# Optimization experiments

Hardware: AMD Instinct MI355X
Metric: run time of the kernel (lower is better)

Reference implementation:

```python
import jax, jax.numpy as jnp
import numpy as np

N_HEAD = 16
NEG = -1e10


def setup_inputs() -> dict:
    key = jax.random.key(0)
    ks = jax.random.split(key, 10)
    B, T, C = 2, 2048, 1024
    hs = C // N_HEAD
    inv = 1.0 / np.sqrt(C)
    return {
        "x": jax.random.normal(ks[0], (B, T, C), jnp.float32),
        "W1": jax.random.normal(ks[1], (C, C), jnp.float32) * inv,
        "bw1": jnp.zeros((C,), jnp.float32),
        "b1": jnp.zeros((hs,), jnp.float32),
        # original init: uniform(-0.001, 0.001)
        "w2": jax.random.uniform(ks[2], (hs, T), jnp.float32, -0.001, 0.001),
        "b2": jnp.zeros((T,), jnp.float32),
        "Wv": jax.random.normal(ks[3], (C, C), jnp.float32) * inv,
        "bv": jnp.zeros((C,), jnp.float32),
        "Wp": jax.random.normal(ks[4], (C, C), jnp.float32) * inv,
        "bp": jnp.zeros((C,), jnp.float32),
    }


def reference(x, W1, bw1, b1, w2, b2, Wv, bv, Wp, bp):
    B, T, C = x.shape
    nh = N_HEAD
    hs = C // nh
    # factorized synthesizer 'query': (B, nh, T, hs)
    h = (x @ W1 + bw1).reshape(B, T, nh, hs).transpose(0, 2, 1, 3)
    # scores: relu(h + b1) @ w2 + b2  -> (B, nh, T, T)
    att = jnp.einsum('bhtd,dk->bhtk', jax.nn.relu(h + b1), w2[:, :T]) + b2[:T]
    # causal mask then softmax (masked_fill with -1e10, as in original)
    causal = jnp.tril(jnp.ones((T, T), bool))
    att = jnp.where(causal[None, None], att, NEG)
    att = jax.nn.softmax(att, axis=-1)
    # values
    v = (x @ Wv + bv).reshape(B, T, nh, hs).transpose(0, 2, 1, 3)
    y = jnp.einsum('bhtk,bhkd->bhtd', att, v)
    y = y.transpose(0, 2, 1, 3).reshape(B, T, C)
    return y @ Wp + bp
```

## Files before the change

kernel.cpp:

```cpp
#include <hip/hip_runtime.h>
#include <hip/hip_bf16.h>

#define TSEQ 2048
#define CDIM 1024
#define NH 16
#define HS 64

typedef __attribute__((ext_vector_type(8))) short bf16x8;
typedef __attribute__((ext_vector_type(4))) float f32x4;
typedef __attribute__((ext_vector_type(16))) float f32x16;

__device__ inline void gload16(const void* g, void* l) {
    __builtin_amdgcn_global_load_lds((const __attribute__((address_space(1))) void*)g,
                                     (__attribute__((address_space(3))) void*)l, 16, 0, 0);
}
__device__ inline void gload4(const void* g, void* l) {
    __builtin_amdgcn_global_load_lds((const __attribute__((address_space(1))) void*)g,
                                     (__attribute__((address_space(3))) void*)l, 4, 0, 0);
}

__device__ inline unsigned packbf(float a, float b) {
    union { __hip_bfloat162 h; unsigned u; } cv;
    cv.h = __float22bfloat162_rn(make_float2(a, b));
    return cv.u;
}

__global__ __launch_bounds__(256)
void prep(const float* __restrict__ x, __hip_bfloat16* __restrict__ xb, int nx,
          const float* __restrict__ W1, const float* __restrict__ Wv,
          const float* __restrict__ Wp, __hip_bfloat16* __restrict__ o1,
          __hip_bfloat16* __restrict__ o2, __hip_bfloat16* __restrict__ o3,
          const float* __restrict__ w2, __hip_bfloat16* __restrict__ w2t,
          const float* __restrict__ b2, float* __restrict__ bl,
          int nconv, int nt3, int nw2)
{
    __shared__ float t[32][33];
    const int bid = blockIdx.x;
    const int tid = threadIdx.x;

    if (bid < nconv) {
        int i = (bid * 256 + tid) * 4;
        if (i + 3 < nx) {
            float4 v = *(const float4*)(x + i);
            union { ushort4 u; __hip_bfloat16 h[4]; } o;
            o.h[0] = __float2bfloat16(v.x);
            o.h[1] = __float2bfloat16(v.y);
            o.h[2] = __float2bfloat16(v.z);
            o.h[3] = __float2bfloat16(v.w);
            *(ushort4*)((unsigned short*)xb + i) = o.u;
        }
    } else if (bid < nconv + nt3) {
        const int idx = bid - nconv;
        const int z = idx >> 10;
        const int rest = idx & 1023;
        const int by = rest >> 5, bx = rest & 31;
        const float* in = z == 0 ? W1 : (z == 1 ? Wv : Wp);
        __hip_bfloat16* out = z == 0 ? o1 : (z == 1 ? o2 : o3);
        const int tx = tid & 31, ty = tid >> 5;
        const int r0 = by * 32, c0 = bx * 32;
        #pragma unroll
        for (int i = 0; i < 32; i += 8)
            t[ty + i][tx] = in[(size_t)(r0 + ty + i) * CDIM + c0 + tx];
        __syncthreads();
        #pragma unroll
        for (int i = 0; i < 32; i += 8)
            out[(size_t)(c0 + ty + i) * CDIM + r0 + tx] = __float2bfloat16(t[tx][ty + i]);
    } else if (bid < nconv + nt3 + nw2) {
        const int idx = bid - nconv - nt3;
        const int bx = idx & 63, by = idx >> 6;
        const int tx = tid & 31, ty = tid >> 5;
        const int r0 = by * 32, c0 = bx * 32;
        #pragma unroll
        for (int i = 0; i < 32; i += 8)
            t[ty + i][tx] = w2[(size_t)(r0 + ty + i) * TSEQ + c0 + tx];
        __syncthreads();
        #pragma unroll
        for (int i = 0; i < 32; i += 8)
            w2t[(size_t)(c0 + ty + i) * HS + r0 + tx] = __float2bfloat16(t[tx][ty + i]);
    } else {
        const int i = (bid - nconv - nt3 - nw2) * 256 + tid;
        if (i < TSEQ) bl[i] = b2[i] * 1.44269504f;
    }
}

__global__ __launch_bounds__(256, 2)
void gemm_qv(const __hip_bfloat16* __restrict__ X, const __hip_bfloat16* __restrict__ W,
             const float* __restrict__ bw1, const float* __restrict__ b1,
             const float* __restrict__ bv, __hip_bfloat16* __restrict__ Hb,
             __hip_bfloat16* __restrict__ Vblk, int M)
{
    __shared__ __align__(16) __hip_bfloat16 As[128 * 32];
    __shared__ __align__(16) __hip_bfloat16 Bs[128 * 32];
    const int tid = threadIdx.x, wave = tid >> 6, lane = tid & 63;
    const int wr = wave >> 1, wc = wave & 1, l15 = lane & 15, l4 = lane >> 4;
    const int m0 = blockIdx.y * 128, n0 = blockIdx.x * 128;
    const int K = CDIM;
    const int Bb = M >> 11;
    const int srow = wave * 32 + (lane >> 2), scol = (lane & 3) * 8;
    const __hip_bfloat16* xg = X + (size_t)(m0 + srow) * K + scol;
    const __hip_bfloat16* wg = W + (size_t)(n0 + srow) * K + scol;
    __hip_bfloat16* la = &As[wave * 32 * 32];
    __hip_bfloat16* lb = &Bs[wave * 32 * 32];

    f32x4 acc[4][4] = {};
    for (int k0 = 0; k0 < K; k0 += 32) {
        __syncthreads();
        gload16(xg + k0, la);
        gload16(xg + k0 + (size_t)16 * K, la + 16 * 32);
        gload16(wg + k0, lb);
        gload16(wg + k0 + (size_t)16 * K, lb + 16 * 32);
        __syncthreads();
        bf16x8 af[4], bfr[4];
        #pragma unroll
        for (int f = 0; f < 4; f++) af[f]  = *(const bf16x8*)&As[(wr * 64 + f * 16 + l15) * 32 + l4 * 8];
        #pragma unroll
        for (int f = 0; f < 4; f++) bfr[f] = *(const bf16x8*)&Bs[(wc * 64 + f * 16 + l15) * 32 + l4 * 8];
        #pragma unroll
        for (int fr = 0; fr < 4; fr++)
            #pragma unroll
            for (int fc = 0; fc < 4; fc++)
                acc[fr][fc] = __builtin_amdgcn_mfma_f32_16x16x32_bf16(af[fr], bfr[fc], acc[fr][fc], 0, 0, 0);
    }

    const bool isH = (n0 < CDIM);
    const int sl4 = ((l4 & 1) << 1) | (l4 >> 1);
    if (isH) {
        #pragma unroll
        for (int fc = 0; fc < 4; fc++) {
            const int col = n0 + wc * 64 + fc * 16 + l15;
            const float bias = bw1[col] + b1[col & (HS - 1)];
            #pragma unroll
            for (int fr = 0; fr < 4; fr++)
                #pragma unroll
                for (int r = 0; r < 4; r++) {
                    const int row = m0 + wr * 64 + fr * 16 + l4 * 4 + r;
                    const float hv = fmaxf(acc[fr][fc][r] + bias, 0.f) * 1.44269504f;
                    Hb[(size_t)row * CDIM + col] = __float2bfloat16(hv);
                }
        }
    } else {
        const int mt = m0 + wr * 64;
        const int bb = mt >> 11;
        const int ktb = (mt & (TSEQ - 1)) >> 6;
        const int hh = ((n0 - CDIM) + wc * 64) >> 6;
        __hip_bfloat16* tile = Vblk + (((size_t)hh * Bb + bb) * (TSEQ / 64) + ktb) * (HS * 64);
        #pragma unroll
        for (int fc = 0; fc < 4; fc++) {
            const int d = fc * 16 + l15;
            const int c2 = hh * HS + d;
            const float bias = bv[c2];
            #pragma unroll
            for (int fr = 0; fr < 4; fr++) {
                const int tl = fr * 16 + sl4 * 4;
                union { ushort4 u; __hip_bfloat16 h[4]; } o;
                #pragma unroll
                for (int r = 0; r < 4; r++) o.h[r] = __float2bfloat16(acc[fr][fc][r] + bias);
                *(ushort4*)(tile + (size_t)d * 64 + tl) = o.u;
            }
        }
    }
}

__global__ __launch_bounds__(256, 2)
void gemm_proj(const __hip_bfloat16* __restrict__ X, const __hip_bfloat16* __restrict__ Wt,
               const float* __restrict__ bN, float* __restrict__ Out, int M)
{
    __shared__ __align__(16) __hip_bfloat16 As[128 * 32];
    __shared__ __align__(16) __hip_bfloat16 Bs[128 * 32];
    const int tid = threadIdx.x, wave = tid >> 6, lane = tid & 63;
    const int wr = wave >> 1, wc = wave & 1, l15 = lane & 15, l4 = lane >> 4;
    const int m0 = blockIdx.y * 128, n0 = blockIdx.x * 128;
    const int K = CDIM;
    const int srow = wave * 32 + (lane >> 2), scol = (lane & 3) * 8;
    const __hip_bfloat16* xg = X + (size_t)(m0 + srow) * K + scol;
    const __hip_bfloat16* wg = Wt + (size_t)(n0 + srow) * K + scol;
    __hip_bfloat16* la = &As[wave * 32 * 32];
    __hip_bfloat16* lb = &Bs[wave * 32 * 32];

    f32x4 acc[4][4] = {};
    for (int k0 = 0; k0 < K; k0 += 32) {
        __syncthreads();
        gload16(xg + k0, la);
        gload16(xg + k0 + (size_t)16 * K, la + 16 * 32);
        gload16(wg + k0, lb);
        gload16(wg + k0 + (size_t)16 * K, lb + 16 * 32);
        __syncthreads();
        bf16x8 af[4], bfr[4];
        #pragma unroll
        for (int f = 0; f < 4; f++) af[f]  = *(const bf16x8*)&As[(wr * 64 + f * 16 + l15) * 32 + l4 * 8];
        #pragma unroll
        for (int f = 0; f < 4; f++) bfr[f] = *(const bf16x8*)&Bs[(wc * 64 + f * 16 + l15) * 32 + l4 * 8];
        #pragma unroll
        for (int fr = 0; fr < 4; fr++)
            #pragma unroll
            for (int fc = 0; fc < 4; fc++)
                acc[fr][fc] = __builtin_amdgcn_mfma_f32_16x16x32_bf16(af[fr], bfr[fc], acc[fr][fc], 0, 0, 0);
    }

    #pragma unroll
    for (int fc = 0; fc < 4; fc++) {
        const int col = n0 + wc * 64 + fc * 16 + l15;
        const float bias = bN[col];
        #pragma unroll
        for (int fr = 0; fr < 4; fr++)
            #pragma unroll
            for (int r = 0; r < 4; r++) {
                const int row = m0 + wr * 64 + fr * 16 + l4 * 4 + r;
                Out[(size_t)row * CDIM + col] = acc[fr][fc][r] + bias;
            }
    }
}

#define STAGE2(KT2, BUF) do {                                                   \
    const size_t tA_ = (size_t)(2 * (KT2)) * (64 * HS);                         \
    const size_t tB_ = (size_t)(2 * (KT2) + 1) * (64 * HS);                     \
    gload16(kg0 + tA_, &Ks[BUF][0][(w * 16) * 64]);                             \
    gload16(kg1 + tA_, &Ks[BUF][0][(w * 16 + 8) * 64]);                         \
    gload16(kg0 + tB_, &Ks[BUF][1][(w * 16) * 64]);                             \
    gload16(kg1 + tB_, &Ks[BUF][1][(w * 16 + 8) * 64]);                         \
    gload16(vg0 + tA_, &Vs[BUF][0][(w * 16) * 64]);                             \
    gload16(vg1 + tA_, &Vs[BUF][0][(w * 16 + 8) * 64]);                         \
    gload16(vg0 + tB_, &Vs[BUF][1][(w * 16) * 64]);                             \
    gload16(vg1 + tB_, &Vs[BUF][1][(w * 16 + 8) * 64]);                         \
    gload4(blg + (size_t)(KT2) * 128, &blr[BUF][0]);                            \
    gload4(blg + (size_t)(KT2) * 128 + 64, &blr[BUF][64]);                      \
} while (0)

__global__ __launch_bounds__(256, 2)
void attn_mfma18(const __hip_bfloat16* __restrict__ H, const __hip_bfloat16* __restrict__ w2t,
                 const __hip_bfloat16* __restrict__ Vblk, const float* __restrict__ bl,
                 __hip_bfloat16* __restrict__ Y, int M)
{
    __shared__ __align__(16) __hip_bfloat16 Ks[2][2][64 * 64];
    __shared__ __align__(16) __hip_bfloat16 Vs[2][2][64 * 64];
    __shared__ __align__(16) float blr[2][128];
    __shared__ float Ls[4 * 32];

    const int tid = threadIdx.x;
    const int w = tid >> 6, lane = tid & 63;
    const int l31 = lane & 31, hi = lane >> 5;
    const int h = blockIdx.y, b = blockIdx.z;
    const int u = (blockIdx.x + blockIdx.y) & 15;
    const int qb = b ? (15 - u) : u;
    const int q0 = qb * 128;
    const int qw = q0 + w * 32;
    const int swz = l31 & 7;
    const int Bb = M >> 11;

    const int srr = lane >> 3, spc = lane & 7;
    const int sr0 = w * 16 + srr, sr1 = sr0 + 8;
    const int sc = (spc ^ srr) * 8;
    const __hip_bfloat16* kg0 = w2t + (size_t)sr0 * HS + sc;
    const __hip_bfloat16* kg1 = w2t + (size_t)sr1 * HS + sc;
    const __hip_bfloat16* vpan = Vblk + (((size_t)h * Bb + b) * (TSEQ / 64)) * (HS * 64);
    const __hip_bfloat16* vg0 = vpan + (size_t)sr0 * 64 + sc;
    const __hip_bfloat16* vg1 = vpan + (size_t)sr1 * 64 + sc;
    const float* blg = bl + lane;

    bf16x8 hf[4];
    {
        const size_t row = (size_t)(b * TSEQ + qw + l31);
        #pragma unroll
        for (int kk = 0; kk < 4; kk++)
            hf[kk] = *(const bf16x8*)(H + row * CDIM + h * HS + kk * 16 + hi * 8);
    }

    f32x16 yA[2] = {};
    f32x16 yB[2] = {};
    float lsA = 0.f, lsB = 0.f;
    const int ntile2 = qb + 1;

    STAGE2(0, 0);

    for (int kt2 = 0; kt2 < ntile2; kt2++) {
        asm volatile("s_waitcnt vmcnt(0)" ::: "memory");
        __builtin_amdgcn_s_barrier();
        __builtin_amdgcn_sched_barrier(0);
        if (kt2 + 1 < ntile2) STAGE2(kt2 + 1, (kt2 + 1) & 1);
        const int buf = kt2 & 1;
        #pragma unroll
        for (int sub = 0; sub < 2; sub++) {
            const int k0 = kt2 * 128 + sub * 64;
            if (k0 > qw + 31) continue;
            const bool nomask = (k0 + 63 <= qw);
            f32x16* yacc = sub ? yB : yA;
            bf16x8 pa[4];
            float lloc = 0.f;
            #pragma unroll
            for (int tf = 0; tf < 2; tf++) {
                f32x16 st;
                #pragma unroll
                for (int g = 0; g < 4; g++) {
                    float4 blv = *(const float4*)&blr[buf][sub * 64 + tf * 32 + g * 8 + hi * 4];
                    st[g * 4 + 0] = blv.x; st[g * 4 + 1] = blv.y;
                    st[g * 4 + 2] = blv.z; st[g * 4 + 3] = blv.w;
                }
                #pragma unroll
                for (int kk = 0; kk < 4; kk++) {
                    const int cs = (kk * 2 + hi) ^ swz;
                    bf16x8 kf = *(const bf16x8*)((const char*)&Ks[buf][sub][0] + (tf * 32 + l31) * 128 + cs * 16);
                    st = __builtin_amdgcn_mfma_f32_32x32x16_bf16(kf, hf[kk], st, 0, 0, 0);
                }
                const int qg = qw + l31;
                float p[16];
                float t0 = 0.f, t1 = 0.f;
                #pragma unroll
                for (int r = 0; r < 16; r++) {
                    float e = __builtin_amdgcn_exp2f(st[r]);
                    if (!nomask) {
                        const int tg = k0 + tf * 32 + (r & 3) + 8 * (r >> 2) + 4 * hi;
                        if (tg > qg) e = 0.f;
                    }
                    p[r] = e;
                    if (r & 1) t1 += e; else t0 += e;
                }
                lloc += t0 + t1;
                #pragma unroll
                for (int m = 0; m < 2; m++) {
                    union { unsigned d[4]; bf16x8 v; } pk;
                    #pragma unroll
                    for (int dw = 0; dw < 4; dw++)
                        pk.d[dw] = packbf(p[8 * m + 2 * dw], p[8 * m + 2 * dw + 1]);
                    pa[tf * 2 + m] = pk.v;
                }
            }
            if (sub) lsB += lloc; else lsA += lloc;
            #pragma unroll
            for (int ks = 0; ks < 4; ks++) {
                const int cs = (ks * 2 + hi) ^ swz;
                #pragma unroll
                for (int df = 0; df < 2; df++) {
                    bf16x8 vf = *(const bf16x8*)((const char*)&Vs[buf][sub][0] + (df * 32 + l31) * 128 + cs * 16);
                    yacc[df] = __builtin_amdgcn_mfma_f32_32x32x16_bf16(pa[ks], vf, yacc[df], 0, 0, 0);
                }
            }
        }
    }
    __syncthreads();

    float lsum = lsA + lsB;
    f32x16 yacc[2];
    yacc[0] = yA[0] + yB[0];
    yacc[1] = yA[1] + yB[1];

    lsum += __shfl_xor(lsum, 32);
    if (hi == 0) Ls[w * 32 + l31] = lsum;
    __syncthreads();

    #pragma unroll
    for (int g = 0; g < 4; g++) {
        float4 lv = *(const float4*)&Ls[w * 32 + g * 8 + hi * 4];
        #pragma unroll
        for (int df = 0; df < 2; df++)
            #pragma unroll
            for (int rr = 0; rr < 4; rr++) {
                const float v = yacc[df][g * 4 + rr] / ((const float*)&lv)[rr];
                const size_t row = (size_t)(b * TSEQ + qw + 8 * g + 4 * hi + rr);
                Y[row * CDIM + h * HS + df * 32 + l31] = __float2bfloat16(v);
            }
    }
}

extern "C" void kernel_launch(void* const* d_in, const int* in_sizes, int n_in,
                              void* d_out, int out_size, void* d_ws, size_t ws_size,
                              hipStream_t stream) {
    const float* x   = (const float*)d_in[0];
    const float* W1  = (const float*)d_in[1];
    const float* bw1 = (const float*)d_in[2];
    const float* b1  = (const float*)d_in[3];
    const float* w2  = (const float*)d_in[4];
    const float* b2  = (const float*)d_in[5];
    const float* Wv  = (const float*)d_in[6];
    const float* bv  = (const float*)d_in[7];
    const float* Wp  = (const float*)d_in[8];
    const float* bp  = (const float*)d_in[9];
    float* out = (float*)d_out;

    const int B = in_sizes[0] / (TSEQ * CDIM);
    const int M = B * TSEQ;
    const size_t MC = (size_t)M * CDIM;
    const size_t WC = (size_t)CDIM * CDIM;

    __hip_bfloat16* xb  = (__hip_bfloat16*)d_ws;
    __hip_bfloat16* Wqv = xb  + MC;
    __hip_bfloat16* Wpt = Wqv + 2 * WC;
    __hip_bfloat16* w2t = Wpt + WC;
    __hip_bfloat16* Hb  = w2t + (size_t)TSEQ * HS;
    __hip_bfloat16* Vbk = Hb  + MC;
    __hip_bfloat16* Yb  = Vbk + MC;
    float*          bl  = (float*)(Yb + MC);

    const int nconv = (int)(MC / 1024);
    const int nt3   = 32 * 32 * 3;
    const int nw2   = (TSEQ / 32) * (HS / 32);
    const int nb2   = TSEQ / 256;

    dim3 blk(256);
    prep<<<dim3(nconv + nt3 + nw2 + nb2), blk, 0, stream>>>(
        x, xb, (int)MC, W1, Wv, Wp, Wqv, Wqv + WC, Wpt, w2, w2t, b2, bl,
        nconv, nt3, nw2);

    gemm_qv<<<dim3(16, M / 128), blk, 0, stream>>>(xb, Wqv, bw1, b1, bv, Hb, Vbk, M);

    attn_mfma18<<<dim3(16, NH, B), blk, 0, stream>>>(Hb, w2t, Vbk, bl, Yb, M);

    gemm_proj<<<dim3(8, M / 128), blk, 0, stream>>>(Yb, Wpt, bp, out, M);
}
```

Baseline: 110.9 us.

## Triple-buffer LDS tiles in QV and projection GEMMs with async prefetch

New measurement: 111.3 us. Within noise of the previous version (+0.4%).

```diff
diff --git a/kernel.cpp b/kernel.cpp
--- a/kernel.cpp
+++ b/kernel.cpp
@@ -83,14 +83,21 @@
     }
 }
 
+#define GSTAGE(K0, BUF) do {                                                    \
+    gload16(xg + (K0), &As[BUF][aoff]);                                         \
+    gload16(xg + (K0) + (size_t)16 * K, &As[BUF][aoff + 16 * 32]);              \
+    gload16(wg + (K0), &Bs[BUF][aoff]);                                         \
+    gload16(wg + (K0) + (size_t)16 * K, &Bs[BUF][aoff + 16 * 32]);              \
+} while (0)
+
 __global__ __launch_bounds__(256, 2)
 void gemm_qv(const __hip_bfloat16* __restrict__ X, const __hip_bfloat16* __restrict__ W,
              const float* __restrict__ bw1, const float* __restrict__ b1,
              const float* __restrict__ bv, __hip_bfloat16* __restrict__ Hb,
              __hip_bfloat16* __restrict__ Vblk, int M)
 {
-    __shared__ __align__(16) __hip_bfloat16 As[128 * 32];
-    __shared__ __align__(16) __hip_bfloat16 Bs[128 * 32];
+    __shared__ __align__(16) __hip_bfloat16 As[3][128 * 32];
+    __shared__ __align__(16) __hip_bfloat16 Bs[3][128 * 32];
     const int tid = threadIdx.x, wave = tid >> 6, lane = tid & 63;
     const int wr = wave >> 1, wc = wave & 1, l15 = lane & 15, l4 = lane >> 4;
     const int m0 = blockIdx.y * 128, n0 = blockIdx.x * 128;
@@ -99,22 +106,24 @@
     const int srow = wave * 32 + (lane >> 2), scol = (lane & 3) * 8;
     const __hip_bfloat16* xg = X + (size_t)(m0 + srow) * K + scol;
     const __hip_bfloat16* wg = W + (size_t)(n0 + srow) * K + scol;
-    __hip_bfloat16* la = &As[wave * 32 * 32];
-    __hip_bfloat16* lb = &Bs[wave * 32 * 32];
+    const int aoff = wave * 32 * 32;
 
     f32x4 acc[4][4] = {};
-    for (int k0 = 0; k0 < K; k0 += 32) {
-        __syncthreads();
-        gload16(xg + k0, la);
-        gload16(xg + k0 + (size_t)16 * K, la + 16 * 32);
-        gload16(wg + k0, lb);
-        gload16(wg + k0 + (size_t)16 * K, lb + 16 * 32);
-        __syncthreads();
+    const int nk = K / 32;
+    GSTAGE(0, 0);
+    GSTAGE(32, 1);
+    for (int ki = 0; ki < nk; ki++) {
+        if (ki + 1 < nk) asm volatile("s_waitcnt vmcnt(4)" ::: "memory");
+        else             asm volatile("s_waitcnt vmcnt(0)" ::: "memory");
+        __builtin_amdgcn_s_barrier();
+        __builtin_amdgcn_sched_barrier(0);
+        if (ki + 2 < nk) GSTAGE((ki + 2) * 32, (ki + 2) % 3);
+        const int buf = ki % 3;
         bf16x8 af[4], bfr[4];
         #pragma unroll
-        for (int f = 0; f < 4; f++) af[f]  = *(const bf16x8*)&As[(wr * 64 + f * 16 + l15) * 32 + l4 * 8];
-        #pragma unroll
-        for (int f = 0; f < 4; f++) bfr[f] = *(const bf16x8*)&Bs[(wc * 64 + f * 16 + l15) * 32 + l4 * 8];
+        for (int f = 0; f < 4; f++) af[f]  = *(const bf16x8*)&As[buf][(wr * 64 + f * 16 + l15) * 32 + l4 * 8];
+        #pragma unroll
+        for (int f = 0; f < 4; f++) bfr[f] = *(const bf16x8*)&Bs[buf][(wc * 64 + f * 16 + l15) * 32 + l4 * 8];
         #pragma unroll
         for (int fr = 0; fr < 4; fr++)
             #pragma unroll
@@ -165,8 +174,8 @@
 void gemm_proj(const __hip_bfloat16* __restrict__ X, const __hip_bfloat16* __restrict__ Wt,
                const float* __restrict__ bN, float* __restrict__ Out, int M)
 {
-    __shared__ __align__(16) __hip_bfloat16 As[128 * 32];
-    __shared__ __align__(16) __hip_bfloat16 Bs[128 * 32];
+    __shared__ __align__(16) __hip_bfloat16 As[3][128 * 32];
+    __shared__ __align__(16) __hip_bfloat16 Bs[3][128 * 32];
     const int tid = threadIdx.x, wave = tid >> 6, lane = tid & 63;
     const int wr = wave >> 1, wc = wave & 1, l15 = lane & 15, l4 = lane >> 4;
     const int m0 = blockIdx.y * 128, n0 = blockIdx.x * 128;
@@ -174,22 +183,24 @@
     const int srow = wave * 32 + (lane >> 2), scol = (lane & 3) * 8;
     const __hip_bfloat16* xg = X + (size_t)(m0 + srow) * K + scol;
     const __hip_bfloat16* wg = Wt + (size_t)(n0 + srow) * K + scol;
-    __hip_bfloat16* la = &As[wave * 32 * 32];
-    __hip_bfloat16* lb = &Bs[wave * 32 * 32];
+    const int aoff = wave * 32 * 32;
 
     f32x4 acc[4][4] = {};
-    for (int k0 = 0; k0 < K; k0 += 32) {
-        __syncthreads();
-        gload16(xg + k0, la);
-        gload16(xg + k0 + (size_t)16 * K, la + 16 * 32);
-        gload16(wg + k0, lb);
-        gload16(wg + k0 + (size_t)16 * K, lb + 16 * 32);
-        __syncthreads();
+    const int nk = K / 32;
+    GSTAGE(0, 0);
+    GSTAGE(32, 1);
+    for (int ki = 0; ki < nk; ki++) {
+        if (ki + 1 < nk) asm volatile("s_waitcnt vmcnt(4)" ::: "memory");
+        else             asm volatile("s_waitcnt vmcnt(0)" ::: "memory");
+        __builtin_amdgcn_s_barrier();
+        __builtin_amdgcn_sched_barrier(0);
+        if (ki + 2 < nk) GSTAGE((ki + 2) * 32, (ki + 2) % 3);
+        const int buf = ki % 3;
         bf16x8 af[4], bfr[4];
         #pragma unroll
-        for (int f = 0; f < 4; f++) af[f]  = *(const bf16x8*)&As[(wr * 64 + f * 16 + l15) * 32 + l4 * 8];
-        #pragma unroll
-        for (int f = 0; f < 4; f++) bfr[f] = *(const bf16x8*)&Bs[(wc * 64 + f * 16 + l15) * 32 + l4 * 8];
+        for (int f = 0; f < 4; f++) af[f]  = *(const bf16x8*)&As[buf][(wr * 64 + f * 16 + l15) * 32 + l4 * 8];
+        #pragma unroll
+        for (int f = 0; f < 4; f++) bfr[f] = *(const bf16x8*)&Bs[buf][(wc * 64 + f * 16 + l15) * 32 + l4 * 8];
         #pragma unroll
         for (int fr = 0; fr < 4; fr++)
             #pragma unroll
```
